# Optimization experiments

Measured on AMD Instinct MI355X. Metric: run time of the kernel, lower is better.

The kernel has to match this reference:

```python
import jax, jax.numpy as jnp
import numpy as np

IO, H, S, N = 64, 1024, 512, 64

def setup_inputs() -> dict:
    key = jax.random.key(0)
    ks = jax.random.split(key, 6)
    scale = 0.05  # keep activations in a sane range for tanh/softmax
    return {
        "states": jax.random.normal(ks[0], (N, S, H), jnp.float32) * scale,
        "output_set": jax.random.normal(ks[1], (IO, H), jnp.float32) * scale,
        "Wo": jax.random.normal(ks[2], (2 * H, H), jnp.float32) * scale,
        "bo": jax.random.normal(ks[3], (H,), jnp.float32) * scale,
        "Wc": jax.random.normal(ks[4], (IO * H, IO), jnp.float32) * scale,
        "bc": jax.random.normal(ks[5], (IO,), jnp.float32) * scale,
    }

def reference(states, output_set, Wo, bo, Wc, bc):
    # Batched over the n_states Python loop of the original module.
    # attn scores: output_set [io,h] x states [n,s,h] -> [n,io,s]
    attn = jnp.einsum('ih,nsh->nis', output_set, states)
    attn = jax.nn.softmax(attn, axis=-1)  # softmax over context (sm_over_context=True)
    mix = jnp.einsum('nis,nsh->nih', attn, states)            # [n,io,h]
    out = jnp.broadcast_to(output_set[None], mix.shape)       # [n,io,h]
    combined = jnp.concatenate([mix, out], axis=-1)           # [n,io,2h]
    o = combined @ Wo + bo                                    # linear_out: 2h -> h
    logits = jnp.tanh(o).reshape(o.shape[0], -1) @ Wc + bc    # C: io*h -> io
    return logits
```

## Files before the change

### kernel.cpp

```cpp
#include <hip/hip_runtime.h>
#include <hip/hip_bf16.h>

#define IOdim 64
#define Hdim  1024
#define Sdim  512
#define Nbat  64

typedef __bf16 bf16x8_t __attribute__((ext_vector_type(8)));
typedef float  f32x4_t  __attribute__((ext_vector_type(4)));

#define MFMA16(a, b, c) __builtin_amdgcn_mfma_f32_16x16x32_bf16((a), (b), (c), 0, 0, 0)

__device__ __forceinline__ unsigned short f2bf(float f) {
    return __builtin_bit_cast(unsigned short, (__bf16)f);
}
__device__ __forceinline__ bf16x8_t cvt8(float4 p0, float4 p1) {
    bf16x8_t b;
    b[0] = (__bf16)p0.x; b[1] = (__bf16)p0.y; b[2] = (__bf16)p0.z; b[3] = (__bf16)p0.w;
    b[4] = (__bf16)p1.x; b[5] = (__bf16)p1.y; b[6] = (__bf16)p1.z; b[7] = (__bf16)p1.w;
    return b;
}
__device__ __forceinline__ void async16(const void* g, void* l) {
    __builtin_amdgcn_global_load_lds(
        (const __attribute__((address_space(1))) void*)g,
        (__attribute__((address_space(3))) void*)l, 16, 0, 0);
}
#define PIPE_SYNC() do { \
    asm volatile("s_waitcnt vmcnt(0)" ::: "memory"); \
    __builtin_amdgcn_s_barrier(); \
} while (0)

__global__ __launch_bounds__(256) void cvt_kernel(const float* __restrict__ in,
                                                  unsigned short* __restrict__ outp,
                                                  int nElem) {
    int idx = blockIdx.x * 256 + threadIdx.x;
    if (idx < nElem) outp[idx] = f2bf(in[idx]);
}

__global__ __launch_bounds__(256) void transpose_cvt(const float* __restrict__ in,
                                                     unsigned short* __restrict__ outp,
                                                     int R, int C) {
    __shared__ float tile[32][33];
    int c0 = blockIdx.x * 32, r0 = blockIdx.y * 32;
    int tx = threadIdx.x, ty = threadIdx.y;
#pragma unroll
    for (int i = 0; i < 4; i++) {
        int r = ty + i * 8;
        tile[r][tx] = in[(size_t)(r0 + r) * C + c0 + tx];
    }
    __syncthreads();
#pragma unroll
    for (int i = 0; i < 4; i++) {
        int r = ty + i * 8;
        outp[(size_t)(c0 + r) * R + r0 + tx] = f2bf(tile[tx][r]);
    }
}

__global__ __launch_bounds__(256) void ob_kernel(const unsigned short* __restrict__ osb,
                                                 const unsigned short* __restrict__ woT,
                                                 const float* __restrict__ bo,
                                                 float* __restrict__ ob) {
    int h0 = blockIdx.x * 64;
    int tid = threadIdx.x, lane = tid & 63, w = tid >> 6;
    int col = lane & 15, quad = lane >> 4;
    f32x4_t acc[4] = {};
    const unsigned short* bp  = woT + (size_t)(h0 + w * 16 + col) * 2048 + 1024 + quad * 8;
    const unsigned short* apb = osb + (size_t)col * 1024 + quad * 8;
    for (int kc = 0; kc < 1024; kc += 32) {
        bf16x8_t bfrag = *(const bf16x8_t*)(bp + kc);
#pragma unroll
        for (int a = 0; a < 4; a++) {
            bf16x8_t afrag = *(const bf16x8_t*)(apb + (size_t)a * 16 * 1024 + kc);
            acc[a] = MFMA16(bfrag, afrag, acc[a]);
        }
    }
#pragma unroll
    for (int a = 0; a < 4; a++)
#pragma unroll
        for (int r = 0; r < 4; r++) {
            int i = a * 16 + col;
            int h = h0 + w * 16 + quad * 4 + r;
            ob[(size_t)i * Hdim + h] = acc[a][r] + bo[h];
        }
}

__global__ __launch_bounds__(256) void scores_kernel(const float* __restrict__ states,
                                                     const unsigned short* __restrict__ osb,
                                                     float* __restrict__ attnf) {
    __shared__ float slab[16 * 1024];
    int n = blockIdx.y, s0 = blockIdx.x * 16;
    int tid = threadIdx.x, lane = tid & 63, w = tid >> 6;
    int col = lane & 15, quad = lane >> 4;
    const float* base = states + ((size_t)(n * Sdim + s0) << 10);
#pragma unroll
    for (int j = 0; j < 16; j++) {
        int swz = (tid & ~15) | ((tid ^ j) & 15);
        async16(base + ((size_t)j << 10) + (swz << 2), slab + j * 1024 + tid * 4);
    }
    PIPE_SYNC();
    const unsigned short* ap = osb + (size_t)(w * 16 + col) * 1024 + quad * 8;
    const float* brow = slab + col * 1024;
    f32x4_t acc = {0, 0, 0, 0};
#pragma unroll 8
    for (int ks = 0; ks < 32; ks++) {
        int sg0 = ks * 8 + quad * 2;
        int p0 = (sg0 & ~15) | ((sg0 ^ col) & 15);
        int p1 = ((sg0 + 1) & ~15) | (((sg0 + 1) ^ col) & 15);
        float4 f0 = *(const float4*)(brow + (p0 << 2));
        float4 f1 = *(const float4*)(brow + (p1 << 2));
        bf16x8_t bfrag = cvt8(f0, f1);
        bf16x8_t afrag = *(const bf16x8_t*)(ap + ks * 32);
        acc = MFMA16(afrag, bfrag, acc);
    }
    float* obp = attnf + (size_t)(n * IOdim + w * 16 + quad * 4) * Sdim + s0 + col;
#pragma unroll
    for (int r = 0; r < 4; r++)
        obp[(size_t)r * Sdim] = acc[r];
}

__global__ __launch_bounds__(256) void softmax_kernel(const float* __restrict__ attnf,
                                                      unsigned short* __restrict__ attnb) {
    int row = blockIdx.x * 4 + (threadIdx.x >> 6);
    int lane = threadIdx.x & 63;
    const float* p = attnf + (size_t)row * Sdim + lane * 8;
    float4 v0 = ((const float4*)p)[0];
    float4 v1 = ((const float4*)p)[1];
    float v[8] = {v0.x, v0.y, v0.z, v0.w, v1.x, v1.y, v1.z, v1.w};
    float m = v[0];
#pragma unroll
    for (int j = 1; j < 8; j++) m = fmaxf(m, v[j]);
#pragma unroll
    for (int off = 32; off > 0; off >>= 1) m = fmaxf(m, __shfl_xor(m, off));
    float sum = 0.f;
#pragma unroll
    for (int j = 0; j < 8; j++) { v[j] = __expf(v[j] - m); sum += v[j]; }
#pragma unroll
    for (int off = 32; off > 0; off >>= 1) sum += __shfl_xor(sum, off);
    float inv = 1.0f / sum;
    union { unsigned short u[8]; uint4 q; } res;
#pragma unroll
    for (int j = 0; j < 8; j++) res.u[j] = f2bf(v[j] * inv);
    *(uint4*)(attnb + (size_t)row * Sdim + lane * 8) = res.q;
}

__global__ __launch_bounds__(256) void mix_kernel(const float* __restrict__ states,
                                                  const unsigned short* __restrict__ attnb,
                                                  unsigned short* __restrict__ mixb) {
    __shared__ unsigned short Tlds[2][64 * 72];
    int n = blockIdx.y, h0 = blockIdx.x * 64;
    int tid = threadIdx.x, lane = tid & 63, g = tid >> 6;
    int col = lane & 15, quad = lane >> 4;
    f32x4_t acc0 = {0,0,0,0}, acc1 = {0,0,0,0}, acc2 = {0,0,0,0}, acc3 = {0,0,0,0};
    const unsigned short* ap = attnb + (size_t)(n * IOdim + col) * Sdim + quad * 8;
    const float* sbase = states + (size_t)n * Sdim * Hdim + h0 + lane;
    float cur[16];
#pragma unroll
    for (int rep = 0; rep < 16; rep++) cur[rep] = sbase[(size_t)(g * 16 + rep) * Hdim];
    for (int t = 0; t < 8; ++t) {
        int sc = t * 64;
        unsigned short* Tb = Tlds[t & 1];
        union { unsigned short u[16]; uint4 q[2]; } pk;
#pragma unroll
        for (int rep = 0; rep < 16; rep++) pk.u[rep] = f2bf(cur[rep]);
        *(uint4*)(Tb + lane * 72 + g * 16)     = pk.q[0];
        *(uint4*)(Tb + lane * 72 + g * 16 + 8) = pk.q[1];
        if (t + 1 < 8) {
#pragma unroll
            for (int rep = 0; rep < 16; rep++)
                cur[rep] = sbase[(size_t)(sc + 64 + g * 16 + rep) * Hdim];
        }
        __syncthreads();
#pragma unroll
        for (int ks = 0; ks < 64; ks += 32) {
            bf16x8_t b  = *(const bf16x8_t*)(Tb + (g * 16 + col) * 72 + ks + quad * 8);
            bf16x8_t a0 = *(const bf16x8_t*)(ap + sc + ks);
            bf16x8_t a1 = *(const bf16x8_t*)(ap + 16 * Sdim + sc + ks);
            bf16x8_t a2 = *(const bf16x8_t*)(ap + 32 * Sdim + sc + ks);
            bf16x8_t a3 = *(const bf16x8_t*)(ap + 48 * Sdim + sc + ks);
            acc0 = MFMA16(a0, b, acc0);
            acc1 = MFMA16(a1, b, acc1);
            acc2 = MFMA16(a2, b, acc2);
            acc3 = MFMA16(a3, b, acc3);
        }
    }
    f32x4_t accs[4] = {acc0, acc1, acc2, acc3};
    int h = h0 + g * 16 + col;
#pragma unroll
    for (int ai = 0; ai < 4; ai++)
#pragma unroll
        for (int r = 0; r < 4; r++) {
            int i = ai * 16 + quad * 4 + r;
            mixb[(size_t)(n * IOdim + i) * Hdim + h] = f2bf(accs[ai][r]);
        }
}

__global__ __launch_bounds__(256) void out_gemm(const unsigned short* __restrict__ mixb,
                                                const unsigned short* __restrict__ woT,
                                                const float* __restrict__ ob,
                                                unsigned short* __restrict__ tb) {
    __shared__ unsigned short Ald[2][128 * 64];
    __shared__ unsigned short Bld[2][64 * 64];
    int h0 = blockIdx.x * 64, r0 = blockIdx.y * 128;
    int tid = threadIdx.x, lane = tid & 63, w = tid >> 6;
    int col = lane & 15, quad = lane >> 4;
    int wx = w & 1, wy = w >> 1;
    int sw = ((tid & 7) ^ ((tid >> 3) & 7)) * 8;
    const unsigned short* m1 = mixb + (size_t)(r0 + (tid >> 3)) * Hdim + sw;
    const unsigned short* w1 = woT + (size_t)(h0 + (tid >> 3)) * 2048 + sw;
    int xs = col & 7;
    unsigned short* A0 = Ald[0]; unsigned short* A1 = Ald[1];
    unsigned short* B0 = Bld[0]; unsigned short* B1 = Bld[1];
    f32x4_t acc[4][2] = {};

#define OG_STAGE(kc, Ab, Bb) do { \
    _Pragma("unroll") for (int j = 0; j < 4; j++) \
        async16(m1 + (size_t)j * 32 * Hdim + (kc), (Ab) + tid * 8 + j * 2048); \
    _Pragma("unroll") for (int j = 0; j < 2; j++) \
        async16(w1 + (size_t)j * 32 * 2048 + (kc), (Bb) + tid * 8 + j * 2048); \
} while (0)

    OG_STAGE(0, A0, B0);
    PIPE_SYNC();
    for (int t = 0; t < 16; ++t) {
        if (t + 1 < 16) OG_STAGE((t + 1) * 64, A1, B1);
#pragma unroll
        for (int kk = 0; kk < 2; kk++) {
            bf16x8_t bfr[2];
#pragma unroll
            for (int ni = 0; ni < 2; ni++)
                bfr[ni] = *(const bf16x8_t*)(B0 + (wx * 32 + ni * 16 + col) * 64
                                             + (((kk * 4 + quad) ^ xs) << 3));
#pragma unroll
            for (int mi = 0; mi < 4; mi++) {
                bf16x8_t af = *(const bf16x8_t*)(A0 + (wy * 64 + mi * 16 + col) * 64
                                                 + (((kk * 4 + quad) ^ xs) << 3));
#pragma unroll
                for (int ni = 0; ni < 2; ni++)
                    acc[mi][ni] = MFMA16(af, bfr[ni], acc[mi][ni]);
            }
        }
        PIPE_SYNC();
        unsigned short* tp;
        tp = A0; A0 = A1; A1 = tp;
        tp = B0; B0 = B1; B1 = tp;
    }
#undef OG_STAGE
#pragma unroll
    for (int ni = 0; ni < 2; ni++) {
        int h = h0 + wx * 32 + ni * 16 + col;
#pragma unroll
        for (int mi = 0; mi < 4; mi++)
#pragma unroll
            for (int r = 0; r < 4; r++) {
                int rr = r0 + wy * 64 + mi * 16 + quad * 4 + r;
                int i = rr & 63;
                tb[(size_t)rr * Hdim + h] = f2bf(tanhf(acc[mi][ni][r] + ob[(size_t)i * Hdim + h]));
            }
    }
}

__global__ __launch_bounds__(256) void final_gemm(const unsigned short* __restrict__ tb,
                                                  const unsigned short* __restrict__ wcT,
                                                  float* __restrict__ partials) {
    __shared__ unsigned short Atile[64 * 256];
    __shared__ unsigned short Btile[64 * 256];
    size_t kb0 = (size_t)blockIdx.x * 512;
    int tid = threadIdx.x, lane = tid & 63, w = tid >> 6;
    int col = lane & 15, quad = lane >> 4;
#pragma unroll
    for (int c = 0; c < 8; c++) {
        int lin = c * 256 + tid;
        int row = lin >> 5, cs = lin & 31;
        int swz = (cs & ~15) | ((cs ^ row) & 15);
        const char* asrc = (const char*)tb  + (size_t)row * 131072 + kb0 + swz * 16;
        const char* bsrc = (const char*)wcT + (size_t)row * 131072 + kb0 + swz * 16;
        async16(asrc, (char*)Atile + lin * 16);
        async16(bsrc, (char*)Btile + lin * 16);
    }
    PIPE_SYNC();
    f32x4_t acc[4] = {};
#pragma unroll
    for (int ks = 0; ks < 8; ks++) {
        int sg = ks * 4 + quad;
        int ph = (sg & ~15) | ((sg ^ col) & 15);
        bf16x8_t bf = *(const bf16x8_t*)(Btile + (w * 16 + col) * 256 + ph * 8);
#pragma unroll
        for (int a = 0; a < 4; a++) {
            bf16x8_t af = *(const bf16x8_t*)(Atile + (a * 16 + col) * 256 + ph * 8);
            acc[a] = MFMA16(af, bf, acc[a]);
        }
    }
    float* pb = partials + (size_t)blockIdx.x * 4096;
    int j = w * 16 + col;
#pragma unroll
    for (int a = 0; a < 4; a++)
#pragma unroll
        for (int r = 0; r < 4; r++) {
            int nn = a * 16 + quad * 4 + r;
            pb[nn * 64 + j] = acc[a][r];
        }
}

__global__ __launch_bounds__(256) void reduce_kernel(const float* __restrict__ partials,
                                                     const float* __restrict__ bc,
                                                     float* __restrict__ out) {
    __shared__ float red[4][64];
    int tid = threadIdx.x, lane = tid & 63, w = tid >> 6;
    int idx = blockIdx.x * 64 + lane;
    float s = 0.f;
#pragma unroll 4
    for (int c = w; c < 256; c += 4) s += partials[(size_t)c * 4096 + idx];
    red[w][lane] = s;
    __syncthreads();
    if (w == 0)
        out[idx] = red[0][lane] + red[1][lane] + red[2][lane] + red[3][lane] + bc[idx & 63];
}

extern "C" void kernel_launch(void* const* d_in, const int* in_sizes, int n_in,
                              void* d_out, int out_size, void* d_ws, size_t ws_size,
                              hipStream_t stream) {
    const float* states     = (const float*)d_in[0];
    const float* output_set = (const float*)d_in[1];
    const float* Wo         = (const float*)d_in[2];
    const float* bo         = (const float*)d_in[3];
    const float* Wc         = (const float*)d_in[4];
    const float* bc         = (const float*)d_in[5];
    float* out = (float*)d_out;

    char* ws = (char*)d_ws;
    float*          attnf = (float*)ws;
    float*          parts = (float*)ws;
    unsigned short* attnb = (unsigned short*)(ws + (8u  << 20));
    unsigned short* mixb  = (unsigned short*)(ws + (12u << 20));
    unsigned short* tb    = (unsigned short*)(ws + (20u << 20));
    unsigned short* woT   = (unsigned short*)(ws + (28u << 20));
    unsigned short* osb   = (unsigned short*)(ws + (32u << 20));
    unsigned short* wcT   = (unsigned short*)(ws + (32u << 20) + (1u << 18));
    float*          obuf  = (float*)(ws + (40u << 20) + (1u << 18));

    cvt_kernel<<<dim3(IOdim * Hdim / 256), dim3(256), 0, stream>>>(output_set, osb, IOdim * Hdim);
    transpose_cvt<<<dim3(Hdim / 32, 2048 / 32), dim3(32, 8), 0, stream>>>(Wo, woT, 2048, Hdim);
    transpose_cvt<<<dim3(64 / 32, 65536 / 32), dim3(32, 8), 0, stream>>>(Wc, wcT, 65536, 64);
    ob_kernel<<<dim3(Hdim / 64), dim3(256), 0, stream>>>(osb, woT, bo, obuf);
    scores_kernel<<<dim3(Sdim / 16, Nbat), dim3(256), 0, stream>>>(states, osb, attnf);
    softmax_kernel<<<dim3(Nbat * IOdim / 4), dim3(256), 0, stream>>>(attnf, attnb);
    mix_kernel<<<dim3(Hdim / 64, Nbat), dim3(256), 0, stream>>>(states, attnb, mixb);
    out_gemm<<<dim3(Hdim / 64, Nbat * IOdim / 128), dim3(256), 0, stream>>>(mixb, woT, obuf, tb);
    final_gemm<<<dim3(256), dim3(256), 0, stream>>>(tb, wcT, parts);
    reduce_kernel<<<dim3(64), dim3(256), 0, stream>>>(parts, bc, out);
}
```

Measured before the change: 332.8 us.

## Merge prep kernels into one launch and replace reduce kernel with atomics

Combines the output_set conversion, both weight transposes, bias initialisation of the output and the ob GEMM into a single prep kernel that dispatches on block index. The ob GEMM now reads fp32 Wo and output_set directly rather than waiting on the converted copies. final_gemm accumulates its partial results into the output with atomicAdd, which removes the partials buffer and the reduce kernel. This saves four kernel launches and the partials round-trip, at the cost of atomic contention from 256 blocks and a summation order that is no longer deterministic. ob is stored transposed so out_gemm reads it contiguously per h.

Result: slower. 350.5 us (+5.3%).

```diff
diff --git a/kernel.cpp b/kernel.cpp
--- a/kernel.cpp
+++ b/kernel.cpp
@@ -30,58 +30,87 @@
     __builtin_amdgcn_s_barrier(); \
 } while (0)
 
-__global__ __launch_bounds__(256) void cvt_kernel(const float* __restrict__ in,
-                                                  unsigned short* __restrict__ outp,
-                                                  int nElem) {
-    int idx = blockIdx.x * 256 + threadIdx.x;
-    if (idx < nElem) outp[idx] = f2bf(in[idx]);
-}
-
-__global__ __launch_bounds__(256) void transpose_cvt(const float* __restrict__ in,
-                                                     unsigned short* __restrict__ outp,
-                                                     int R, int C) {
-    __shared__ float tile[32][33];
-    int c0 = blockIdx.x * 32, r0 = blockIdx.y * 32;
-    int tx = threadIdx.x, ty = threadIdx.y;
-#pragma unroll
-    for (int i = 0; i < 4; i++) {
-        int r = ty + i * 8;
-        tile[r][tx] = in[(size_t)(r0 + r) * C + c0 + tx];
-    }
-    __syncthreads();
-#pragma unroll
-    for (int i = 0; i < 4; i++) {
-        int r = ty + i * 8;
-        outp[(size_t)(c0 + r) * R + r0 + tx] = f2bf(tile[tx][r]);
-    }
-}
-
-__global__ __launch_bounds__(256) void ob_kernel(const unsigned short* __restrict__ osb,
-                                                 const unsigned short* __restrict__ woT,
-                                                 const float* __restrict__ bo,
-                                                 float* __restrict__ ob) {
-    int h0 = blockIdx.x * 64;
-    int tid = threadIdx.x, lane = tid & 63, w = tid >> 6;
-    int col = lane & 15, quad = lane >> 4;
-    f32x4_t acc[4] = {};
-    const unsigned short* bp  = woT + (size_t)(h0 + w * 16 + col) * 2048 + 1024 + quad * 8;
-    const unsigned short* apb = osb + (size_t)col * 1024 + quad * 8;
-    for (int kc = 0; kc < 1024; kc += 32) {
-        bf16x8_t bfrag = *(const bf16x8_t*)(bp + kc);
-#pragma unroll
-        for (int a = 0; a < 4; a++) {
-            bf16x8_t afrag = *(const bf16x8_t*)(apb + (size_t)a * 16 * 1024 + kc);
-            acc[a] = MFMA16(bfrag, afrag, acc[a]);
-        }
-    }
-#pragma unroll
-    for (int a = 0; a < 4; a++)
-#pragma unroll
-        for (int r = 0; r < 4; r++) {
-            int i = a * 16 + col;
-            int h = h0 + w * 16 + quad * 4 + r;
-            ob[(size_t)i * Hdim + h] = acc[a][r] + bo[h];
-        }
+__global__ __launch_bounds__(256) void prep_kernel(
+    const float* __restrict__ output_set, const float* __restrict__ Wo,
+    const float* __restrict__ Wc, const float* __restrict__ bo,
+    const float* __restrict__ bc,
+    unsigned short* __restrict__ osb, unsigned short* __restrict__ woT,
+    unsigned short* __restrict__ wcT, float* __restrict__ obT,
+    float* __restrict__ out) {
+    __shared__ __align__(16) char smem[10240];
+    int b = blockIdx.x, tid = threadIdx.x;
+    if (b < 16) {
+        int base = b * 4096 + tid;
+#pragma unroll
+        for (int it = 0; it < 16; it++)
+            osb[base + it * 256] = f2bf(output_set[base + it * 256]);
+    } else if (b < 6160) {
+        const float* in; unsigned short* outp; int R, C, bx, by;
+        if (b < 2064) {
+            in = Wo; outp = woT; R = 2048; C = 1024;
+            int bb = b - 16; bx = bb & 31; by = bb >> 5;
+        } else {
+            in = Wc; outp = wcT; R = 65536; C = 64;
+            int bb = b - 2064; bx = bb & 1; by = bb >> 1;
+        }
+        float (*tile)[33] = (float (*)[33])smem;
+        int c0 = bx * 32, r0 = by * 32;
+        int tx = tid & 31, ty = tid >> 5;
+#pragma unroll
+        for (int i = 0; i < 4; i++) {
+            int r = ty + i * 8;
+            tile[r][tx] = in[(size_t)(r0 + r) * C + c0 + tx];
+        }
+        __syncthreads();
+#pragma unroll
+        for (int i = 0; i < 4; i++) {
+            int r = ty + i * 8;
+            outp[(size_t)(c0 + r) * R + r0 + tx] = f2bf(tile[tx][r]);
+        }
+    } else if (b == 6160) {
+#pragma unroll
+        for (int it = 0; it < 16; it++) {
+            int idx = it * 256 + tid;
+            out[idx] = bc[idx & 63];
+        }
+    } else {
+        unsigned short* Tl = (unsigned short*)smem;
+        int h0 = (b - 6161) * 64;
+        int lane = tid & 63, g = tid >> 6, col = lane & 15, quad = lane >> 4;
+        const float* wbase = Wo + (size_t)1024 * 1024 + h0 + lane;
+        f32x4_t acc[4] = {};
+        for (int t = 0; t < 16; ++t) {
+            int k0 = t * 64;
+            float cur[16];
+#pragma unroll
+            for (int rep = 0; rep < 16; rep++)
+                cur[rep] = wbase[(size_t)(k0 + g * 16 + rep) * 1024];
+            union { unsigned short u[16]; uint4 q[2]; } pk;
+#pragma unroll
+            for (int rep = 0; rep < 16; rep++) pk.u[rep] = f2bf(cur[rep]);
+            if (t) __syncthreads();
+            *(uint4*)(Tl + lane * 72 + g * 16)     = pk.q[0];
+            *(uint4*)(Tl + lane * 72 + g * 16 + 8) = pk.q[1];
+            __syncthreads();
+#pragma unroll
+            for (int ks = 0; ks < 64; ks += 32) {
+                bf16x8_t wf = *(const bf16x8_t*)(Tl + (g * 16 + col) * 72 + ks + quad * 8);
+#pragma unroll
+                for (int ai = 0; ai < 4; ai++) {
+                    const float* osp = output_set + (size_t)(ai * 16 + col) * 1024 + k0 + ks + quad * 8;
+                    bf16x8_t of = cvt8(*(const float4*)osp, *(const float4*)(osp + 4));
+                    acc[ai] = MFMA16(wf, of, acc[ai]);
+                }
+            }
+        }
+#pragma unroll
+        for (int ai = 0; ai < 4; ai++)
+#pragma unroll
+            for (int r = 0; r < 4; r++) {
+                int h = h0 + g * 16 + quad * 4 + r;
+                obT[(size_t)h * 64 + ai * 16 + col] = acc[ai][r] + bo[h];
+            }
+    }
 }
 
 __global__ __launch_bounds__(256) void scores_kernel(const float* __restrict__ states,
@@ -196,7 +225,7 @@
 
 __global__ __launch_bounds__(256) void out_gemm(const unsigned short* __restrict__ mixb,
                                                 const unsigned short* __restrict__ woT,
-                                                const float* __restrict__ ob,
+                                                const float* __restrict__ obT,
                                                 unsigned short* __restrict__ tb) {
     __shared__ unsigned short Ald[2][128 * 64];
     __shared__ unsigned short Bld[2][64 * 64];
@@ -248,20 +277,21 @@
 #pragma unroll
     for (int ni = 0; ni < 2; ni++) {
         int h = h0 + wx * 32 + ni * 16 + col;
+        const float* obp = obT + (size_t)h * 64;
 #pragma unroll
         for (int mi = 0; mi < 4; mi++)
 #pragma unroll
             for (int r = 0; r < 4; r++) {
                 int rr = r0 + wy * 64 + mi * 16 + quad * 4 + r;
                 int i = rr & 63;
-                tb[(size_t)rr * Hdim + h] = f2bf(tanhf(acc[mi][ni][r] + ob[(size_t)i * Hdim + h]));
+                tb[(size_t)rr * Hdim + h] = f2bf(tanhf(acc[mi][ni][r] + obp[i]));
             }
     }
 }
 
 __global__ __launch_bounds__(256) void final_gemm(const unsigned short* __restrict__ tb,
                                                   const unsigned short* __restrict__ wcT,
-                                                  float* __restrict__ partials) {
+                                                  float* __restrict__ out) {
     __shared__ unsigned short Atile[64 * 256];
     __shared__ unsigned short Btile[64 * 256];
     size_t kb0 = (size_t)blockIdx.x * 512;
@@ -290,30 +320,14 @@
             acc[a] = MFMA16(af, bf, acc[a]);
         }
     }
-    float* pb = partials + (size_t)blockIdx.x * 4096;
     int j = w * 16 + col;
 #pragma unroll
     for (int a = 0; a < 4; a++)
 #pragma unroll
         for (int r = 0; r < 4; r++) {
             int nn = a * 16 + quad * 4 + r;
-            pb[nn * 64 + j] = acc[a][r];
-        }
-}
-
-__global__ __launch_bounds__(256) void reduce_kernel(const float* __restrict__ partials,
-                                                     const float* __restrict__ bc,
-                                                     float* __restrict__ out) {
-    __shared__ float red[4][64];
-    int tid = threadIdx.x, lane = tid & 63, w = tid >> 6;
-    int idx = blockIdx.x * 64 + lane;
-    float s = 0.f;
-#pragma unroll 4
-    for (int c = w; c < 256; c += 4) s += partials[(size_t)c * 4096 + idx];
-    red[w][lane] = s;
-    __syncthreads();
-    if (w == 0)
-        out[idx] = red[0][lane] + red[1][lane] + red[2][lane] + red[3][lane] + bc[idx & 63];
+            atomicAdd(out + nn * 64 + j, acc[a][r]);
+        }
 }
 
 extern "C" void kernel_launch(void* const* d_in, const int* in_sizes, int n_in,
@@ -329,23 +343,19 @@
 
     char* ws = (char*)d_ws;
     float*          attnf = (float*)ws;
-    float*          parts = (float*)ws;
     unsigned short* attnb = (unsigned short*)(ws + (8u  << 20));
     unsigned short* mixb  = (unsigned short*)(ws + (12u << 20));
     unsigned short* tb    = (unsigned short*)(ws + (20u << 20));
     unsigned short* woT   = (unsigned short*)(ws + (28u << 20));
     unsigned short* osb   = (unsigned short*)(ws + (32u << 20));
     unsigned short* wcT   = (unsigned short*)(ws + (32u << 20) + (1u << 18));
-    float*          obuf  = (float*)(ws + (40u << 20) + (1u << 18));
-
-    cvt_kernel<<<dim3(IOdim * Hdim / 256), dim3(256), 0, stream>>>(output_set, osb, IOdim * Hdim);
-    transpose_cvt<<<dim3(Hdim / 32, 2048 / 32), dim3(32, 8), 0, stream>>>(Wo, woT, 2048, Hdim);
-    transpose_cvt<<<dim3(64 / 32, 65536 / 32), dim3(32, 8), 0, stream>>>(Wc, wcT, 65536, 64);
-    ob_kernel<<<dim3(Hdim / 64), dim3(256), 0, stream>>>(osb, woT, bo, obuf);
+    float*          obT   = (float*)(ws + (40u << 20) + (1u << 18));
+
+    prep_kernel<<<dim3(6177), dim3(256), 0, stream>>>(output_set, Wo, Wc, bo, bc,
+                                                      osb, woT, wcT, obT, out);
     scores_kernel<<<dim3(Sdim / 16, Nbat), dim3(256), 0, stream>>>(states, osb, attnf);
     softmax_kernel<<<dim3(Nbat * IOdim / 4), dim3(256), 0, stream>>>(attnf, attnb);
     mix_kernel<<<dim3(Hdim / 64, Nbat), dim3(256), 0, stream>>>(states, attnb, mixb);
-    out_gemm<<<dim3(Hdim / 64, Nbat * IOdim / 128), dim3(256), 0, stream>>>(mixb, woT, obuf, tb);
-    final_gemm<<<dim3(256), dim3(256), 0, stream>>>(tb, wcT, parts);
-    reduce_kernel<<<dim3(64), dim3(256), 0, stream>>>(parts, bc, out);
-}
+    out_gemm<<<dim3(Hdim / 64, Nbat * IOdim / 128), dim3(256), 0, stream>>>(mixb, woT, obT, tb);
+    final_gemm<<<dim3(256), dim3(256), 0, stream>>>(tb, wcT, out);
+}
```
